# Kernel tuning notes

Measured on AMD Instinct MI355X. Metric: run time of the kernel, lower is better.

Reference implementation:

```python
import jax, jax.numpy as jnp
import numpy as np

N_LAYERS = 3
NUM_NODES = 400000
EMB_DIM = 64
N_EDGES = 4000000


def setup_inputs() -> dict:
    key = jax.random.key(0)
    k1, k2, k3, k4 = jax.random.split(key, 4)
    embedding = jax.random.normal(k1, (NUM_NODES, EMB_DIM), dtype=jnp.float32) * 0.1
    adj_row = jax.random.randint(k2, (N_EDGES,), 0, NUM_NODES, dtype=jnp.int64)
    adj_col = jax.random.randint(k3, (N_EDGES,), 0, NUM_NODES, dtype=jnp.int64)
    # normalized adjacency values (e.g. 1/sqrt(d_i d_j)); positive, small
    adj_val = jax.random.uniform(k4, (N_EDGES,), dtype=jnp.float32) * 0.01
    return {"embedding": embedding, "adj_row": adj_row, "adj_col": adj_col, "adj_val": adj_val}


def _spmm(row, col, val, x):
    # sparse [N,N] @ dense [N,D]: gather neighbor rows, scale, scatter-add
    msgs = val[:, None] * x[col]                      # [E, D]
    return jax.ops.segment_sum(msgs, row, num_segments=NUM_NODES)


def reference(embedding, adj_row, adj_col, adj_val):
    # LightGCN propagation: running mean over layer outputs (fused accumulator,
    # mathematically identical to stack+mean over n_layers+1 embeddings)
    x = embedding
    acc = x
    for _ in range(N_LAYERS):
        x = _spmm(adj_row, adj_col, adj_val, x)
        acc = acc + x
    all_embeddings = acc / jnp.asarray(N_LAYERS + 1, dtype=x.dtype)
    return all_embeddings
```

## Files before the change

### kernel.cpp

```cpp
#include <hip/hip_runtime.h>

#define EMB 64
#define SCAN_B 256

typedef unsigned uint2v __attribute__((ext_vector_type(2)));
typedef float float4v __attribute__((ext_vector_type(4)));

__device__ inline uint2 nt_load_u2(const uint2* p) {
    uint2v v = __builtin_nontemporal_load((const uint2v*)p);
    return make_uint2(v.x, v.y);
}
__device__ inline void nt_store_u2(uint2* p, uint2 v) {
    uint2v t; t.x = v.x; t.y = v.y;
    __builtin_nontemporal_store(t, (uint2v*)p);
}
__device__ inline float4 nt_load_f4(const float4* p) {
    float4v v = __builtin_nontemporal_load((const float4v*)p);
    return make_float4(v.x, v.y, v.z, v.w);
}
__device__ inline void nt_store_f4(float4* p, float4 v) {
    float4v t; t.x = v.x; t.y = v.y; t.z = v.z; t.w = v.w;
    __builtin_nontemporal_store(t, (float4v*)p);
}

__device__ inline unsigned short f2bf(float f) {
    unsigned u = __float_as_uint(f);
    return (unsigned short)((u + 0x7fffu + ((u >> 16) & 1u)) >> 16);
}
__device__ inline float bl(unsigned u) { return __uint_as_float(u << 16); }
__device__ inline float bh(unsigned u) { return __uint_as_float(u & 0xffff0000u); }


__global__ void zero_ints(int* __restrict__ p, int n) {
    int i = blockIdx.x * blockDim.x + threadIdx.x;
    if (i < n) p[i] = 0;
}

__global__ void hist_rows(const int* __restrict__ row, int* __restrict__ S, int E) {
    int e = blockIdx.x * blockDim.x + threadIdx.x;
    if (e < E) atomicAdd(&S[__builtin_nontemporal_load(row + e)], 1);
}

__global__ void scan_block_sums(const int* __restrict__ S, int* __restrict__ bsum, int N) {
    __shared__ int sdata[SCAN_B];
    int i = blockIdx.x * SCAN_B + threadIdx.x;
    sdata[threadIdx.x] = (i < N) ? S[i] : 0;
    __syncthreads();
    for (int off = SCAN_B / 2; off > 0; off >>= 1) {
        if (threadIdx.x < off) sdata[threadIdx.x] += sdata[threadIdx.x + off];
        __syncthreads();
    }
    if (threadIdx.x == 0) bsum[blockIdx.x] = sdata[0];
}

__global__ void scan_sums(int* __restrict__ bsum, int nb) {
    __shared__ int part[1024];
    int t = threadIdx.x;
    int i0 = 2 * t, i1 = 2 * t + 1;
    int a = (i0 < nb) ? bsum[i0] : 0;
    int b = (i1 < nb) ? bsum[i1] : 0;
    part[t] = a + b;
    __syncthreads();
    for (int off = 1; off < 1024; off <<= 1) {
        int v = part[t];
        int add = (t >= off) ? part[t - off] : 0;
        __syncthreads();
        part[t] = v + add;
        __syncthreads();
    }
    int excl = (t == 0) ? 0 : part[t - 1];
    if (i0 < nb) bsum[i0] = excl;
    if (i1 < nb) bsum[i1] = excl + a;
}

__global__ void scan_apply(int* __restrict__ S, const int* __restrict__ bsum, int N) {
    __shared__ int sdata[SCAN_B];
    int i = blockIdx.x * SCAN_B + threadIdx.x;
    int v = (i < N) ? S[i] : 0;
    sdata[threadIdx.x] = v;
    __syncthreads();
    for (int off = 1; off < SCAN_B; off <<= 1) {
        int val = sdata[threadIdx.x];
        int add = (threadIdx.x >= off) ? sdata[threadIdx.x - off] : 0;
        __syncthreads();
        sdata[threadIdx.x] = val + add;
        __syncthreads();
    }
    int excl = (threadIdx.x == 0 ? 0 : sdata[threadIdx.x - 1]) + bsum[blockIdx.x];
    if (i < N) S[i] = excl;
}

__global__ void scatter_edges_ranged(const int* __restrict__ row, const int* __restrict__ col,
                                     const float* __restrict__ val,
                                     int* __restrict__ S, uint2* __restrict__ epack,
                                     int E, int rstep) {
    int pass  = blockIdx.x & 7;
    int chunk = blockIdx.x >> 3;
    int e = chunk * blockDim.x + threadIdx.x;
    if (e >= E) return;
    int r = __builtin_nontemporal_load(row + e);
    int lo = pass * rstep;
    if (r < lo || r >= lo + rstep) return;
    int c = __builtin_nontemporal_load(col + e);
    float v = __builtin_nontemporal_load(val + e);
    int pos = atomicAdd(&S[r], 1);
    epack[pos] = make_uint2((unsigned)c, __float_as_uint(v));
}

__global__ void conv_bf16(const float4* __restrict__ src, uint2* __restrict__ dst, int n4) {
    int i = blockIdx.x * blockDim.x + threadIdx.x;
    if (i < n4) {
        float4 v = nt_load_f4(src + i);
        unsigned w0 = (unsigned)f2bf(v.x) | ((unsigned)f2bf(v.y) << 16);
        unsigned w1 = (unsigned)f2bf(v.z) | ((unsigned)f2bf(v.w) << 16);
        nt_store_u2(dst + i, make_uint2(w0, w1));
    }
}

__global__ void spmm_csr(const uint2* __restrict__ epack, const int* __restrict__ S,
                         const unsigned short* __restrict__ x, const float* __restrict__ emb,
                         unsigned short* __restrict__ y, float* __restrict__ acc,
                         int N, int mode) {
    int r = (blockIdx.x * blockDim.x + threadIdx.x) >> 6;
    if (r >= N) return;
    int lane = threadIdx.x & 63;
    int grp = lane >> 4;
    int d4  = lane & 15;

    int beg = (r == 0) ? 0 : S[r - 1];
    int end = S[r];

    float4 s = make_float4(0.f, 0.f, 0.f, 0.f);
    const uint2 z2 = make_uint2(0u, 0u);

    for (int base = beg; base < end; base += 16) {
        uint2 p0 = z2, p1 = z2, p2 = z2, p3 = z2;
        int i0 = base + grp, i1 = i0 + 4, i2 = i0 + 8, i3 = i0 + 12;
        if (i0 < end) p0 = nt_load_u2(epack + i0);
        if (i1 < end) p1 = nt_load_u2(epack + i1);
        if (i2 < end) p2 = nt_load_u2(epack + i2);
        if (i3 < end) p3 = nt_load_u2(epack + i3);
        uint2 g0 = (i0 < end) ? ((const uint2*)(x + ((size_t)p0.x << 6)))[d4] : z2;
        uint2 g1 = (i1 < end) ? ((const uint2*)(x + ((size_t)p1.x << 6)))[d4] : z2;
        uint2 g2 = (i2 < end) ? ((const uint2*)(x + ((size_t)p2.x << 6)))[d4] : z2;
        uint2 g3 = (i3 < end) ? ((const uint2*)(x + ((size_t)p3.x << 6)))[d4] : z2;
        float w0 = (i0 < end) ? __uint_as_float(p0.y) : 0.f;
        float w1 = (i1 < end) ? __uint_as_float(p1.y) : 0.f;
        float w2 = (i2 < end) ? __uint_as_float(p2.y) : 0.f;
        float w3 = (i3 < end) ? __uint_as_float(p3.y) : 0.f;
        s.x += w0 * bl(g0.x); s.y += w0 * bh(g0.x); s.z += w0 * bl(g0.y); s.w += w0 * bh(g0.y);
        s.x += w1 * bl(g1.x); s.y += w1 * bh(g1.x); s.z += w1 * bl(g1.y); s.w += w1 * bh(g1.y);
        s.x += w2 * bl(g2.x); s.y += w2 * bh(g2.x); s.z += w2 * bl(g2.y); s.w += w2 * bh(g2.y);
        s.x += w3 * bl(g3.x); s.y += w3 * bh(g3.x); s.z += w3 * bl(g3.y); s.w += w3 * bh(g3.y);
    }

    s.x += __shfl_xor(s.x, 32); s.y += __shfl_xor(s.y, 32);
    s.z += __shfl_xor(s.z, 32); s.w += __shfl_xor(s.w, 32);
    s.x += __shfl_xor(s.x, 16); s.y += __shfl_xor(s.y, 16);
    s.z += __shfl_xor(s.z, 16); s.w += __shfl_xor(s.w, 16);

    if (lane < 16) {
        size_t o4 = (size_t)r * 16 + d4;
        if (mode != 2) {
            unsigned w0 = (unsigned)f2bf(s.x) | ((unsigned)f2bf(s.y) << 16);
            unsigned w1 = (unsigned)f2bf(s.z) | ((unsigned)f2bf(s.w) << 16);
            nt_store_u2(((uint2*)y) + o4, make_uint2(w0, w1));
        }
        if (mode == 0) {
            float4 e4 = nt_load_f4(((const float4*)emb) + o4);
            nt_store_f4(((float4*)acc) + o4,
                        make_float4(e4.x+s.x, e4.y+s.y, e4.z+s.z, e4.w+s.w));
        } else if (mode == 1) {
            float4 a4 = nt_load_f4(((const float4*)acc) + o4);
            nt_store_f4(((float4*)acc) + o4,
                        make_float4(a4.x+s.x, a4.y+s.y, a4.z+s.z, a4.w+s.w));
        } else {
            float4 a4 = nt_load_f4(((const float4*)acc) + o4);
            nt_store_f4(((float4*)acc) + o4,
                        make_float4((a4.x+s.x)*0.25f, (a4.y+s.y)*0.25f,
                                    (a4.z+s.z)*0.25f, (a4.w+s.w)*0.25f));
        }
    }
}


__global__ void lgcn_init(const float4* __restrict__ emb, float4* __restrict__ A,
                          float4* __restrict__ acc, float4* __restrict__ B, int n4) {
    int i = blockIdx.x * blockDim.x + threadIdx.x;
    if (i < n4) { float4 v = emb[i]; A[i] = v; acc[i] = v; B[i] = make_float4(0,0,0,0); }
}
__global__ void lgcn_spmm(const int* __restrict__ row, const int* __restrict__ col,
                          const float* __restrict__ val, const float* __restrict__ x,
                          float* __restrict__ y, int E) {
    int gid = blockIdx.x * blockDim.x + threadIdx.x;
    int e = gid >> 6;
    if (e >= E) return;
    int d = threadIdx.x & 63;
    atomicAdd(y + (size_t)row[e] * EMB + d, val[e] * x[(size_t)col[e] * EMB + d]);
}
__global__ void lgcn_addzero(float4* __restrict__ acc, const float4* __restrict__ X,
                             float4* __restrict__ Y, int n4) {
    int i = blockIdx.x * blockDim.x + threadIdx.x;
    if (i < n4) {
        float4 a = acc[i]; float4 xv = X[i];
        a.x += xv.x; a.y += xv.y; a.z += xv.z; a.w += xv.w;
        acc[i] = a; Y[i] = make_float4(0,0,0,0);
    }
}
__global__ void lgcn_final(float4* __restrict__ acc, const float4* __restrict__ X, int n4) {
    int i = blockIdx.x * blockDim.x + threadIdx.x;
    if (i < n4) {
        float4 a = acc[i]; float4 xv = X[i];
        a.x = (a.x + xv.x) * 0.25f; a.y = (a.y + xv.y) * 0.25f;
        a.z = (a.z + xv.z) * 0.25f; a.w = (a.w + xv.w) * 0.25f;
        acc[i] = a;
    }
}

extern "C" void kernel_launch(void* const* d_in, const int* in_sizes, int n_in,
                              void* d_out, int out_size, void* d_ws, size_t ws_size,
                              hipStream_t stream) {
    const float* emb = (const float*)d_in[0];
    const int*   row = (const int*)d_in[1];
    const int*   col = (const int*)d_in[2];
    const float* val = (const float*)d_in[3];
    float* acc = (float*)d_out;

    const int N = in_sizes[0] / EMB;
    const int E = in_sizes[1];
    const int TB = 256;

    const size_t buf_elems = (size_t)N * EMB;
    const int nb = (N + SCAN_B - 1) / SCAN_B;

    const size_t need = (size_t)E * 8 + buf_elems * 2 * 3 + (size_t)N * 4 + (size_t)nb * 4;

    if (ws_size >= need) {
        uint2* epack = (uint2*)d_ws;
        unsigned short* X0 = (unsigned short*)(epack + E);
        unsigned short* X1 = X0 + buf_elems;
        unsigned short* X2 = X1 + buf_elems;
        int* S    = (int*)(X2 + buf_elems);
        int* bsum = S + N;

        const int eb  = (E + TB - 1) / TB;
        const int nbN = (N + TB - 1) / TB;
        const int n4  = (int)(buf_elems / 4);
        const int cvb = (n4 + TB - 1) / TB;
        const int spmm_blocks = (N + 3) / 4;
        const int rstep = (N + 7) / 8;

        zero_ints<<<nbN, TB, 0, stream>>>(S, N);
        hist_rows<<<eb, TB, 0, stream>>>(row, S, E);
        scan_block_sums<<<nb, SCAN_B, 0, stream>>>(S, bsum, N);
        scan_sums<<<1, 1024, 0, stream>>>(bsum, nb);
        scan_apply<<<nb, SCAN_B, 0, stream>>>(S, bsum, N);
        scatter_edges_ranged<<<eb * 8, TB, 0, stream>>>(row, col, val, S, epack, E, rstep);
        conv_bf16<<<cvb, TB, 0, stream>>>((const float4*)emb, (uint2*)X0, n4);

        spmm_csr<<<spmm_blocks, TB, 0, stream>>>(epack, S, X0, emb, X1, acc, N, 0);
        spmm_csr<<<spmm_blocks, TB, 0, stream>>>(epack, S, X1, nullptr, X2, acc, N, 1);
        spmm_csr<<<spmm_blocks, TB, 0, stream>>>(epack, S, X2, nullptr, nullptr, acc, N, 2);
    } else {
        float* A = (float*)d_ws;
        float* B = A + buf_elems;
        const int n4 = (int)(buf_elems / 4);
        const int ew_blocks = (n4 + TB - 1) / TB;
        const int spmm_blocks = (E + 3) / 4;
        lgcn_init<<<ew_blocks, TB, 0, stream>>>((const float4*)emb, (float4*)A,
                                                (float4*)acc, (float4*)B, n4);
        lgcn_spmm<<<spmm_blocks, TB, 0, stream>>>(row, col, val, A, B, E);
        lgcn_addzero<<<ew_blocks, TB, 0, stream>>>((float4*)acc, (const float4*)B,
                                                   (float4*)A, n4);
        lgcn_spmm<<<spmm_blocks, TB, 0, stream>>>(row, col, val, B, A, E);
        lgcn_addzero<<<ew_blocks, TB, 0, stream>>>((float4*)acc, (const float4*)A,
                                                   (float4*)B, n4);
        lgcn_spmm<<<spmm_blocks, TB, 0, stream>>>(row, col, val, A, B, E);
        lgcn_final<<<ew_blocks, TB, 0, stream>>>((float4*)acc, (const float4*)B, n4);
    }
}
```

Baseline: 1.197 ms.

## Process multiple rows per wave with LDS-staged edges and next-row prefetch

```diff
diff --git a/kernel.cpp b/kernel.cpp
--- a/kernel.cpp
+++ b/kernel.cpp
@@ -2,6 +2,9 @@
 
 #define EMB 64
 #define SCAN_B 256
+#define RPB 32
+#define RPW 8
+#define ECAP 1024
 
 typedef unsigned uint2v __attribute__((ext_vector_type(2)));
 typedef float float4v __attribute__((ext_vector_type(4)));
@@ -117,70 +120,146 @@
     }
 }
 
-__global__ void spmm_csr(const uint2* __restrict__ epack, const int* __restrict__ S,
-                         const unsigned short* __restrict__ x, const float* __restrict__ emb,
-                         unsigned short* __restrict__ y, float* __restrict__ acc,
-                         int N, int mode) {
-    int r = (blockIdx.x * blockDim.x + threadIdx.x) >> 6;
-    if (r >= N) return;
-    int lane = threadIdx.x & 63;
-    int grp = lane >> 4;
-    int d4  = lane & 15;
-
-    int beg = (r == 0) ? 0 : S[r - 1];
-    int end = S[r];
-
-    float4 s = make_float4(0.f, 0.f, 0.f, 0.f);
+template<bool STG>
+__device__ __forceinline__ void spmm_rows(
+    const uint2* __restrict__ epack, const uint2* __restrict__ esh, int beg0,
+    const int* __restrict__ Ssh, int j0,
+    const unsigned short* __restrict__ x, const float* __restrict__ emb,
+    unsigned short* __restrict__ y, float* __restrict__ acc,
+    int rb, int N, int mode, int lane, int grp, int d4)
+{
     const uint2 z2 = make_uint2(0u, 0u);
 
-    for (int base = beg; base < end; base += 16) {
-        uint2 p0 = z2, p1 = z2, p2 = z2, p3 = z2;
-        int i0 = base + grp, i1 = i0 + 4, i2 = i0 + 8, i3 = i0 + 12;
-        if (i0 < end) p0 = nt_load_u2(epack + i0);
-        if (i1 < end) p1 = nt_load_u2(epack + i1);
-        if (i2 < end) p2 = nt_load_u2(epack + i2);
-        if (i3 < end) p3 = nt_load_u2(epack + i3);
-        uint2 g0 = (i0 < end) ? ((const uint2*)(x + ((size_t)p0.x << 6)))[d4] : z2;
-        uint2 g1 = (i1 < end) ? ((const uint2*)(x + ((size_t)p1.x << 6)))[d4] : z2;
-        uint2 g2 = (i2 < end) ? ((const uint2*)(x + ((size_t)p2.x << 6)))[d4] : z2;
-        uint2 g3 = (i3 < end) ? ((const uint2*)(x + ((size_t)p3.x << 6)))[d4] : z2;
-        float w0 = (i0 < end) ? __uint_as_float(p0.y) : 0.f;
-        float w1 = (i1 < end) ? __uint_as_float(p1.y) : 0.f;
-        float w2 = (i2 < end) ? __uint_as_float(p2.y) : 0.f;
-        float w3 = (i3 < end) ? __uint_as_float(p3.y) : 0.f;
-        s.x += w0 * bl(g0.x); s.y += w0 * bh(g0.x); s.z += w0 * bl(g0.y); s.w += w0 * bh(g0.y);
-        s.x += w1 * bl(g1.x); s.y += w1 * bh(g1.x); s.z += w1 * bl(g1.y); s.w += w1 * bh(g1.y);
-        s.x += w2 * bl(g2.x); s.y += w2 * bh(g2.x); s.z += w2 * bl(g2.y); s.w += w2 * bh(g2.y);
-        s.x += w3 * bl(g3.x); s.y += w3 * bh(g3.x); s.z += w3 * bl(g3.y); s.w += w3 * bh(g3.y);
-    }
-
-    s.x += __shfl_xor(s.x, 32); s.y += __shfl_xor(s.y, 32);
-    s.z += __shfl_xor(s.z, 32); s.w += __shfl_xor(s.w, 32);
-    s.x += __shfl_xor(s.x, 16); s.y += __shfl_xor(s.y, 16);
-    s.z += __shfl_xor(s.z, 16); s.w += __shfl_xor(s.w, 16);
-
-    if (lane < 16) {
-        size_t o4 = (size_t)r * 16 + d4;
-        if (mode != 2) {
-            unsigned w0 = (unsigned)f2bf(s.x) | ((unsigned)f2bf(s.y) << 16);
-            unsigned w1 = (unsigned)f2bf(s.z) | ((unsigned)f2bf(s.w) << 16);
-            nt_store_u2(((uint2*)y) + o4, make_uint2(w0, w1));
+#define EDG(i) (STG ? esh[(i) - beg0] : epack[i])
+#define LOADR(J, B_, E_, P0, P1, P2, P3, G0, G1, G2, G3)                         \
+    {                                                                            \
+        B_ = Ssh[J]; E_ = Ssh[(J) + 1];                                          \
+        int i0 = B_ + grp, i1 = i0 + 4, i2 = i0 + 8, i3 = i0 + 12;               \
+        P0 = (i0 < E_) ? EDG(i0) : z2;                                           \
+        P1 = (i1 < E_) ? EDG(i1) : z2;                                           \
+        P2 = (i2 < E_) ? EDG(i2) : z2;                                           \
+        P3 = (i3 < E_) ? EDG(i3) : z2;                                           \
+        G0 = (i0 < E_) ? ((const uint2*)(x + ((size_t)P0.x << 6)))[d4] : z2;     \
+        G1 = (i1 < E_) ? ((const uint2*)(x + ((size_t)P1.x << 6)))[d4] : z2;     \
+        G2 = (i2 < E_) ? ((const uint2*)(x + ((size_t)P2.x << 6)))[d4] : z2;     \
+        G3 = (i3 < E_) ? ((const uint2*)(x + ((size_t)P3.x << 6)))[d4] : z2;     \
+    }
+
+    int aB = 0, aE = 0;
+    uint2 ap0 = z2, ap1 = z2, ap2 = z2, ap3 = z2, ag0 = z2, ag1 = z2, ag2 = z2, ag3 = z2;
+    int bB = 0, bE = 0;
+    uint2 bp0 = z2, bp1 = z2, bp2 = z2, bp3 = z2, bg0 = z2, bg1 = z2, bg2 = z2, bg3 = z2;
+
+    LOADR(j0, aB, aE, ap0, ap1, ap2, ap3, ag0, ag1, ag2, ag3);
+
+    for (int k = 0; k < RPW; ++k) {
+        int j = j0 + k;
+        int r = rb + j;
+        if (k + 1 < RPW) {
+            LOADR(j + 1, bB, bE, bp0, bp1, bp2, bp3, bg0, bg1, bg2, bg3);
         }
-        if (mode == 0) {
-            float4 e4 = nt_load_f4(((const float4*)emb) + o4);
-            nt_store_f4(((float4*)acc) + o4,
-                        make_float4(e4.x+s.x, e4.y+s.y, e4.z+s.z, e4.w+s.w));
-        } else if (mode == 1) {
-            float4 a4 = nt_load_f4(((const float4*)acc) + o4);
-            nt_store_f4(((float4*)acc) + o4,
-                        make_float4(a4.x+s.x, a4.y+s.y, a4.z+s.z, a4.w+s.w));
-        } else {
-            float4 a4 = nt_load_f4(((const float4*)acc) + o4);
-            nt_store_f4(((float4*)acc) + o4,
-                        make_float4((a4.x+s.x)*0.25f, (a4.y+s.y)*0.25f,
-                                    (a4.z+s.z)*0.25f, (a4.w+s.w)*0.25f));
+
+        float4 s = make_float4(0.f, 0.f, 0.f, 0.f);
+        {
+            int i0 = aB + grp, i1 = i0 + 4, i2 = i0 + 8, i3 = i0 + 12;
+            float w0 = (i0 < aE) ? __uint_as_float(ap0.y) : 0.f;
+            float w1 = (i1 < aE) ? __uint_as_float(ap1.y) : 0.f;
+            float w2 = (i2 < aE) ? __uint_as_float(ap2.y) : 0.f;
+            float w3 = (i3 < aE) ? __uint_as_float(ap3.y) : 0.f;
+            s.x += w0 * bl(ag0.x); s.y += w0 * bh(ag0.x); s.z += w0 * bl(ag0.y); s.w += w0 * bh(ag0.y);
+            s.x += w1 * bl(ag1.x); s.y += w1 * bh(ag1.x); s.z += w1 * bl(ag1.y); s.w += w1 * bh(ag1.y);
+            s.x += w2 * bl(ag2.x); s.y += w2 * bh(ag2.x); s.z += w2 * bl(ag2.y); s.w += w2 * bh(ag2.y);
+            s.x += w3 * bl(ag3.x); s.y += w3 * bh(ag3.x); s.z += w3 * bl(ag3.y); s.w += w3 * bh(ag3.y);
         }
-    }
+        for (int base = aB + 16; base < aE; base += 16) {
+            int i0 = base + grp, i1 = i0 + 4, i2 = i0 + 8, i3 = i0 + 12;
+            uint2 p0 = (i0 < aE) ? EDG(i0) : z2;
+            uint2 p1 = (i1 < aE) ? EDG(i1) : z2;
+            uint2 p2 = (i2 < aE) ? EDG(i2) : z2;
+            uint2 p3 = (i3 < aE) ? EDG(i3) : z2;
+            uint2 g0 = (i0 < aE) ? ((const uint2*)(x + ((size_t)p0.x << 6)))[d4] : z2;
+            uint2 g1 = (i1 < aE) ? ((const uint2*)(x + ((size_t)p1.x << 6)))[d4] : z2;
+            uint2 g2 = (i2 < aE) ? ((const uint2*)(x + ((size_t)p2.x << 6)))[d4] : z2;
+            uint2 g3 = (i3 < aE) ? ((const uint2*)(x + ((size_t)p3.x << 6)))[d4] : z2;
+            float w0 = (i0 < aE) ? __uint_as_float(p0.y) : 0.f;
+            float w1 = (i1 < aE) ? __uint_as_float(p1.y) : 0.f;
+            float w2 = (i2 < aE) ? __uint_as_float(p2.y) : 0.f;
+            float w3 = (i3 < aE) ? __uint_as_float(p3.y) : 0.f;
+            s.x += w0 * bl(g0.x); s.y += w0 * bh(g0.x); s.z += w0 * bl(g0.y); s.w += w0 * bh(g0.y);
+            s.x += w1 * bl(g1.x); s.y += w1 * bh(g1.x); s.z += w1 * bl(g1.y); s.w += w1 * bh(g1.y);
+            s.x += w2 * bl(g2.x); s.y += w2 * bh(g2.x); s.z += w2 * bl(g2.y); s.w += w2 * bh(g2.y);
+            s.x += w3 * bl(g3.x); s.y += w3 * bh(g3.x); s.z += w3 * bl(g3.y); s.w += w3 * bh(g3.y);
+        }
+
+        s.x += __shfl_xor(s.x, 32); s.y += __shfl_xor(s.y, 32);
+        s.z += __shfl_xor(s.z, 32); s.w += __shfl_xor(s.w, 32);
+        s.x += __shfl_xor(s.x, 16); s.y += __shfl_xor(s.y, 16);
+        s.z += __shfl_xor(s.z, 16); s.w += __shfl_xor(s.w, 16);
+
+        if (lane < 16 && r < N) {
+            size_t o4 = (size_t)r * 16 + d4;
+            if (mode != 2) {
+                unsigned w0 = (unsigned)f2bf(s.x) | ((unsigned)f2bf(s.y) << 16);
+                unsigned w1 = (unsigned)f2bf(s.z) | ((unsigned)f2bf(s.w) << 16);
+                nt_store_u2(((uint2*)y) + o4, make_uint2(w0, w1));
+            }
+            if (mode == 0) {
+                float4 e4 = nt_load_f4(((const float4*)emb) + o4);
+                nt_store_f4(((float4*)acc) + o4,
+                            make_float4(e4.x + s.x, e4.y + s.y, e4.z + s.z, e4.w + s.w));
+            } else if (mode == 1) {
+                float4 a4 = nt_load_f4(((const float4*)acc) + o4);
+                nt_store_f4(((float4*)acc) + o4,
+                            make_float4(a4.x + s.x, a4.y + s.y, a4.z + s.z, a4.w + s.w));
+            } else if (mode == 2) {
+                float4 a4 = nt_load_f4(((const float4*)acc) + o4);
+                nt_store_f4(((float4*)acc) + o4,
+                            make_float4((a4.x + s.x) * 0.25f, (a4.y + s.y) * 0.25f,
+                                        (a4.z + s.z) * 0.25f, (a4.w + s.w) * 0.25f));
+            }
+        }
+        aB = bB; aE = bE;
+        ap0 = bp0; ap1 = bp1; ap2 = bp2; ap3 = bp3;
+        ag0 = bg0; ag1 = bg1; ag2 = bg2; ag3 = bg3;
+    }
+#undef LOADR
+#undef EDG
+}
+
+__global__ __launch_bounds__(256) void spmm_csr2(
+    const uint2* __restrict__ epack, const int* __restrict__ S,
+    const unsigned short* __restrict__ x, const float* __restrict__ emb,
+    unsigned short* __restrict__ y, float* __restrict__ acc,
+    int N, int mode)
+{
+    __shared__ int Ssh[RPB + 1];
+    __shared__ uint2 esh[ECAP];
+
+    int tid = threadIdx.x;
+    int rb = blockIdx.x * RPB;
+
+    if (tid <= RPB) {
+        int rr = rb - 1 + tid;
+        Ssh[tid] = (rr < 0) ? 0 : S[rr < N ? rr : (N - 1)];
+    }
+    __syncthreads();
+
+    int beg0 = Ssh[0];
+    int nE = Ssh[RPB] - beg0;
+    bool staged = (nE <= ECAP);
+    if (staged) {
+        for (int i = tid; i < nE; i += 256) esh[i] = nt_load_u2(epack + beg0 + i);
+    }
+    __syncthreads();
+
+    int wid = tid >> 6, lane = tid & 63;
+    int grp = lane >> 4, d4 = lane & 15;
+    int j0 = wid * RPW;
+
+    if (staged)
+        spmm_rows<true >(epack, esh, beg0, Ssh, j0, x, emb, y, acc, rb, N, mode, lane, grp, d4);
+    else
+        spmm_rows<false>(epack, esh, beg0, Ssh, j0, x, emb, y, acc, rb, N, mode, lane, grp, d4);
 }
 
 
@@ -247,7 +326,7 @@
         const int nbN = (N + TB - 1) / TB;
         const int n4  = (int)(buf_elems / 4);
         const int cvb = (n4 + TB - 1) / TB;
-        const int spmm_blocks = (N + 3) / 4;
+        const int spmm_blocks = (N + RPB - 1) / RPB;
         const int rstep = (N + 7) / 8;
 
         zero_ints<<<nbN, TB, 0, stream>>>(S, N);
@@ -258,9 +337,9 @@
         scatter_edges_ranged<<<eb * 8, TB, 0, stream>>>(row, col, val, S, epack, E, rstep);
         conv_bf16<<<cvb, TB, 0, stream>>>((const float4*)emb, (uint2*)X0, n4);
 
-        spmm_csr<<<spmm_blocks, TB, 0, stream>>>(epack, S, X0, emb, X1, acc, N, 0);
-        spmm_csr<<<spmm_blocks, TB, 0, stream>>>(epack, S, X1, nullptr, X2, acc, N, 1);
-        spmm_csr<<<spmm_blocks, TB, 0, stream>>>(epack, S, X2, nullptr, nullptr, acc, N, 2);
+        spmm_csr2<<<spmm_blocks, TB, 0, stream>>>(epack, S, X0, emb, X1, acc, N, 0);
+        spmm_csr2<<<spmm_blocks, TB, 0, stream>>>(epack, S, X1, nullptr, X2, acc, N, 1);
+        spmm_csr2<<<spmm_blocks, TB, 0, stream>>>(epack, S, X2, nullptr, nullptr, acc, N, 2);
     } else {
         float* A = (float*)d_ws;
         float* B = A + buf_elems;
```

Measured after the change: 1.050 ms. 1.14x faster.
